# Optimization experiments

Hardware: AMD Instinct MI355X
Metric: run time of the kernel (lower is better)

Reference implementation:

```python
import jax, jax.numpy as jnp
import numpy as np

TOK_DIM, POS_DIM, HEAD_DIM = 3, 3, 64
D_MODEL, T, B = 128, 4096, 8


def setup_inputs() -> dict:
    key = jax.random.key(0)
    ks = jax.random.split(key, 8)
    s = 0.1
    return {
        "x": jax.random.normal(ks[0], (B, T, TOK_DIM + POS_DIM), jnp.float32),
        "Wq1": jax.random.normal(ks[1], (TOK_DIM, HEAD_DIM), jnp.float32) * s,
        "Wk1": jax.random.normal(ks[2], (TOK_DIM, HEAD_DIM), jnp.float32) * s,
        "Wv1": jax.random.normal(ks[3], (TOK_DIM, HEAD_DIM), jnp.float32) * s,
        "Wq2": jax.random.normal(ks[4], (POS_DIM, HEAD_DIM), jnp.float32) * s,
        "Wk2": jax.random.normal(ks[5], (POS_DIM, HEAD_DIM), jnp.float32) * s,
        "Wv2": jax.random.normal(ks[6], (POS_DIM, HEAD_DIM), jnp.float32) * s,
        "Wout": jax.random.normal(ks[7], (2 * HEAD_DIM, D_MODEL), jnp.float32) * s,
    }


def _attend(q, k, v):
    # q,k,v: [B,T,HEAD_DIM]; causal scaled dot-product attention
    scale = 1.0 / np.sqrt(HEAD_DIM).astype(np.float32)
    scores = jnp.einsum('btd,bsd->bts', q, k) * scale  # [B,T,T]
    t = scores.shape[1]
    causal = jnp.arange(t)[:, None] >= jnp.arange(t)[None, :]
    scores = jnp.where(causal[None], scores, -jnp.inf)
    p = jax.nn.softmax(scores, axis=-1)
    return jnp.einsum('bts,bsd->btd', p, v)


def reference(x, Wq1, Wk1, Wv1, Wq2, Wk2, Wv2, Wout):
    x_tok = x[:, :, :TOK_DIM]
    x_pos = x[:, :, TOK_DIM:]
    out1 = _attend(x_tok @ Wq1, x_tok @ Wk1, x_tok @ Wv1)
    out2 = _attend(x_pos @ Wq2, x_pos @ Wk2, x_pos @ Wv2)
    out = jnp.concatenate([out1, out2], axis=-1)  # [B,T,2*HEAD_DIM]
    return out @ Wout  # [B,T,D_MODEL]
```

## Files before the change

### kernel.cpp

```cpp
#include <hip/hip_runtime.h>
#include <hip/hip_bf16.h>
#include <stdint.h>

#define T_SEQ 4096

typedef float  f32x4   __attribute__((ext_vector_type(4)));
typedef float  f32x16  __attribute__((ext_vector_type(16)));
typedef short  bf16x8  __attribute__((ext_vector_type(8)));
typedef unsigned int u32x4 __attribute__((ext_vector_type(4)));

typedef const __attribute__((address_space(1))) uint32_t* gptr_t;
typedef __attribute__((address_space(3))) uint32_t* lptr_t;

__device__ __forceinline__ uint32_t f2bf1(float f) {
    uint32_t u = __float_as_uint(f);
    return (u + 0x7fffu + ((u >> 16) & 1u)) >> 16;
}
__device__ __forceinline__ short f2bfs(float f) { return (short)f2bf1(f); }
__device__ __forceinline__ uint32_t cvtpk(float lo, float hi) {
    uint32_t r;
    asm("v_cvt_pk_bf16_f32 %0, %1, %2" : "=v"(r) : "v"(lo), "v"(hi));
    return r;
}

__global__ __launch_bounds__(256) void qk_proj(
    const float* __restrict__ x,
    const float* __restrict__ Wq1, const float* __restrict__ Wk1,
    const float* __restrict__ Wq2, const float* __restrict__ Wk2,
    short* __restrict__ Q, short* __restrict__ K)
{
    int idx = blockIdx.x * 256 + threadIdx.x;
    int d = idx & 63;
    int t = (idx >> 6) & (T_SEQ - 1);
    int b = idx >> 18;
    const float* xp = x + (size_t)(b * T_SEQ + t) * 6;
    float x0 = xp[0], x1 = xp[1], x2 = xp[2];
    float x3 = xp[3], x4 = xp[4], x5 = xp[5];
    const float QS = 0.125f * 1.44269504088896340736f;
    float q1 = (x0 * Wq1[d] + x1 * Wq1[64 + d] + x2 * Wq1[128 + d]) * QS;
    float k1 =  x0 * Wk1[d] + x1 * Wk1[64 + d] + x2 * Wk1[128 + d];
    float q2 = (x3 * Wq2[d] + x4 * Wq2[64 + d] + x5 * Wq2[128 + d]) * QS;
    float k2 =  x3 * Wk2[d] + x4 * Wk2[64 + d] + x5 * Wk2[128 + d];
    size_t base1 = ((size_t)(b * 2 + 0) * T_SEQ + t) * 64 + d;
    size_t base2 = ((size_t)(b * 2 + 1) * T_SEQ + t) * 64 + d;
    Q[base1] = f2bfs(q1);  Q[base2] = f2bfs(q2);
    K[base1] = f2bfs(k1);  K[base2] = f2bfs(k2);
}

__global__ __launch_bounds__(256) void v_proj_t(
    const float* __restrict__ x,
    const float* __restrict__ Wv1, const float* __restrict__ Wv2,
    short* __restrict__ Vt)
{
    int bh = blockIdx.x >> 6;
    int tt = blockIdx.x & 63;
    int head = bh & 1, b = bh >> 1;
    int t  = tt * 64 + (threadIdx.x & 63);
    int dg = threadIdx.x >> 6;
    const float* Wv = head ? Wv2 : Wv1;
    const float* xp = x + (size_t)(b * T_SEQ + t) * 6 + head * 3;
    float x0 = xp[0], x1 = xp[1], x2 = xp[2];
    size_t base = (size_t)bh * 64 * T_SEQ + t;
    #pragma unroll
    for (int k = 0; k < 16; ++k) {
        int d = dg * 16 + k;
        float v = x0 * Wv[d] + x1 * Wv[64 + d] + x2 * Wv[128 + d];
        Vt[base + (size_t)d * T_SEQ] = f2bfs(v);
    }
}

__global__ __launch_bounds__(256, 4) void attn(
    const short* __restrict__ Q, const short* __restrict__ K,
    const short* __restrict__ Vt, float* __restrict__ Hf,
    float* __restrict__ P1, float* __restrict__ L0, float* __restrict__ L1)
{
    __shared__ __align__(16) char smem[32768];

    int id = blockIdx.x;
    int xcd = id & 7, rest = id >> 3;
    int bh = xcd * 2 + (rest & 1);
    int rem = rest >> 1;
    int s  = 63 - (rem >> 1);
    int p  = rem & 1;
    int tid = threadIdx.x;
    int W = tid >> 6;
    int lane = tid & 63;
    int ql = lane & 31, h = lane >> 5;
    int tile = W >> 1, half = W & 1;
    int t0 = 64 * s + 32 * tile;
    int q  = t0 + ql;
    int n  = s + 1;
    int nb = (n - p + 1) >> 1;

    size_t kvbase = (size_t)bh * (T_SEQ * 64);

    bf16x8 qf[4];
    #pragma unroll
    for (int ks = 0; ks < 4; ++ks)
        qf[ks] = *(const bf16x8*)(Q + kvbase + (size_t)q * 64 + ks * 16 + h * 8);

    int krl = tid >> 3;
    int kcol = ((tid & 7) ^ (krl & 7)) * 8;
    const short* ksrc0 = K + kvbase + kcol;
    const short* vsrc0 = Vt + kvbase + kcol;

    f32x16 acc0, acc1;
    #pragma unroll
    for (int rr = 0; rr < 16; ++rr) { acc0[rr] = 0.f; acc1[rr] = 0.f; }
    float l = 0.f;
    int swz = (ql & 7) << 4;

#define STAGE(bsel, kvv)                                                        \
    {                                                                           \
        char* kb = smem + (bsel) * 16384;                                       \
        char* vb = kb + 8192;                                                   \
        _Pragma("unroll")                                                       \
        for (int z = 0; z < 2; ++z)                                             \
            __builtin_amdgcn_global_load_lds(                                   \
                (gptr_t)(ksrc0 + (size_t)((kvv) + 32 * z + krl) * 64),          \
                (lptr_t)(kb + z * 4096 + tid * 16), 16, 0, 0);                  \
        _Pragma("unroll")                                                       \
        for (int z = 0; z < 2; ++z)                                             \
            __builtin_amdgcn_global_load_lds(                                   \
                (gptr_t)(vsrc0 + (size_t)(32 * z + krl) * T_SEQ + (kvv)),       \
                (lptr_t)(vb + z * 4096 + tid * 16), 16, 0, 0);                  \
    }

#define QK_SM(pf0, pf1)                                                         \
        {                                                                       \
            f32x16 Sv;                                                          \
            _Pragma("unroll") for (int rr = 0; rr < 16; ++rr) Sv[rr] = 0.f;     \
            Sv = __builtin_amdgcn_mfma_f32_32x32x16_bf16(kf0, qf[0], Sv,0,0,0); \
            Sv = __builtin_amdgcn_mfma_f32_32x32x16_bf16(kf1, qf[1], Sv,0,0,0); \
            Sv = __builtin_amdgcn_mfma_f32_32x32x16_bf16(kf2, qf[2], Sv,0,0,0); \
            Sv = __builtin_amdgcn_mfma_f32_32x32x16_bf16(kf3, qf[3], Sv,0,0,0); \
            bool needmask = (kv0 + 32 * half + 31 > t0);       \
            uint32_t pw[8];                                                     \
            float l0 = 0.f, l1 = 0.f;                                           \
            _Pragma("unroll") for (int e = 0; e < 8; ++e) {                     \
                float p0 = __builtin_amdgcn_exp2f(Sv[2 * e]);                   \
                float p1 = __builtin_amdgcn_exp2f(Sv[2 * e + 1]);               \
                if (needmask) {                                                 \
                    int kv = kv0 + 32 * half + 4 * h + 2 * (e & 1) + 8 * (e >> 1); \
                    p0 = (kv     <= q) ? p0 : 0.f;                              \
                    p1 = (kv + 1 <= q) ? p1 : 0.f;                              \
                }                                                               \
                l0 += p0; l1 += p1;                                             \
                pw[e] = cvtpk(p0, p1);                                          \
            }                                                                   \
            l += l0 + l1;                                                       \
            {                                                                   \
                uint32_t a0 = pw[0], b0 = pw[2], a1 = pw[1], b1 = pw[3];        \
                asm("v_permlane32_swap_b32 %0, %1" : "+v"(a0), "+v"(b0));       \
                asm("v_permlane32_swap_b32 %0, %1" : "+v"(a1), "+v"(b1));       \
                u32x4 fr = {a0, a1, b0, b1};                                    \
                pf0 = __builtin_bit_cast(bf16x8, fr);                           \
                uint32_t c0 = pw[4], d0 = pw[6], c1 = pw[5], d1 = pw[7];        \
                asm("v_permlane32_swap_b32 %0, %1" : "+v"(c0), "+v"(d0));       \
                asm("v_permlane32_swap_b32 %0, %1" : "+v"(c1), "+v"(d1));       \
                u32x4 fr1 = {c0, c1, d0, d1};                                   \
                pf1 = __builtin_bit_cast(bf16x8, fr1);                          \
            }                                                                   \
        }

#define BODY(jj)                                                                \
    {                                                                           \
        const int kv0 = 64 * (p + 2 * (jj));                                    \
        if ((jj) + 1 < nb) STAGE(((jj) + 1) & 1, kv0 + 128);                    \
        const char* kb = smem + ((jj) & 1) * 16384;                             \
        const char* vb = kb + 8192;                                             \
        const char* krw = kb + (32 * half + ql) * 128;                          \
        bf16x8 kf0 = *(const bf16x8*)(krw + ((0 * 32 + h * 16) ^ swz));         \
        bf16x8 kf1 = *(const bf16x8*)(krw + ((1 * 32 + h * 16) ^ swz));         \
        bf16x8 kf2 = *(const bf16x8*)(krw + ((2 * 32 + h * 16) ^ swz));         \
        bf16x8 kf3 = *(const bf16x8*)(krw + ((3 * 32 + h * 16) ^ swz));         \
        bool act = (kv0 + 32 * half <= t0 + 31);                                \
        bf16x8 pf0, pf1;                                                        \
        __builtin_amdgcn_s_setprio(1);                                          \
        if (act) QK_SM(pf0, pf1)                                                \
        const char* vr0 = vb + ql * 128;                                        \
        const char* vr1 = vb + (32 + ql) * 128;                                 \
        int vc0 = (64 * half + 16 * h) ^ swz;                                   \
        int vc1 = (64 * half + 32 + 16 * h) ^ swz;                              \
        bf16x8 vf00 = *(const bf16x8*)(vr0 + vc0);                              \
        bf16x8 vf01 = *(const bf16x8*)(vr0 + vc1);                              \
        bf16x8 vf10 = *(const bf16x8*)(vr1 + vc0);                              \
        bf16x8 vf11 = *(const bf16x8*)(vr1 + vc1);                              \
        if (act) {                                                              \
            acc0 = __builtin_amdgcn_mfma_f32_32x32x16_bf16(vf00, pf0, acc0, 0, 0, 0); \
            acc0 = __builtin_amdgcn_mfma_f32_32x32x16_bf16(vf01, pf1, acc0, 0, 0, 0); \
            acc1 = __builtin_amdgcn_mfma_f32_32x32x16_bf16(vf10, pf0, acc1, 0, 0, 0); \
            acc1 = __builtin_amdgcn_mfma_f32_32x32x16_bf16(vf11, pf1, acc1, 0, 0, 0); \
        }                                                                       \
        __builtin_amdgcn_s_setprio(0);                                          \
        __syncthreads();                                                        \
    }

    if (nb > 0) STAGE(0, 64 * p);
    __syncthreads();

    for (int j = 0; j < nb; ++j) BODY(j);
#undef BODY
#undef QK_SM
#undef STAGE

    l += __shfl_xor(l, 32);
    float* sg = (float*)smem + tile * 2112 + lane * 33;
    if (half == 1) {
        #pragma unroll
        for (int g = 0; g < 4; ++g) {
            *(f32x4*)(sg + 4 * g)      = f32x4{acc0[4*g+0], acc0[4*g+1], acc0[4*g+2], acc0[4*g+3]};
            *(f32x4*)(sg + 16 + 4 * g) = f32x4{acc1[4*g+0], acc1[4*g+1], acc1[4*g+2], acc1[4*g+3]};
        }
        sg[32] = l;
    }
    __syncthreads();
    if (half == 0) {
        #pragma unroll
        for (int g = 0; g < 4; ++g) {
            f32x4 u0 = *(f32x4*)(sg + 4 * g);
            f32x4 u1 = *(f32x4*)(sg + 16 + 4 * g);
            acc0[4*g+0] += u0[0]; acc0[4*g+1] += u0[1]; acc0[4*g+2] += u0[2]; acc0[4*g+3] += u0[3];
            acc1[4*g+0] += u1[0]; acc1[4*g+1] += u1[1]; acc1[4*g+2] += u1[2]; acc1[4*g+3] += u1[3];
        }
        l += sg[32];
        int head = bh & 1, bb = bh >> 1;
        float* Pdst = p ? P1 : Hf;
        float* Ldst = p ? L1 : L0;
        float* hp = Pdst + ((size_t)(bb * T_SEQ) + t0 + ql) * 128 + head * 64 + 4 * h;
        #pragma unroll
        for (int g2 = 0; g2 < 4; ++g2) {
            f32x4 s0 = { acc0[g2*4+0], acc0[g2*4+1], acc0[g2*4+2], acc0[g2*4+3] };
            *(f32x4*)(hp + 8 * g2) = s0;
            f32x4 s1 = { acc1[g2*4+0], acc1[g2*4+1], acc1[g2*4+2], acc1[g2*4+3] };
            *(f32x4*)(hp + 32 + 8 * g2) = s1;
        }
        if (h == 0)
            Ldst[(size_t)bh * T_SEQ + t0 + ql] = l;
    }
}

__global__ __launch_bounds__(256) void prep_wt(
    const float* __restrict__ Wout, short* __restrict__ Wt)
{
    int tid = blockIdx.x * 256 + threadIdx.x;
    int j = tid >> 7, k = tid & 127;
    float v = Wout[k * 128 + j];
    int slot = k >> 3;
    Wt[j * 128 + (((slot ^ (j & 7)) << 3) | (k & 7))] = f2bfs(v);
}

__global__ __launch_bounds__(256) void out_proj(
    const float* P0, const float* __restrict__ P1,
    const float* __restrict__ L0, const float* __restrict__ L1,
    const short* __restrict__ Wt, float* out)
{
    __shared__ __align__(16) char lws[32768];
    int tid = threadIdx.x;
    int w = tid >> 6, lane = tid & 63, c = lane & 15, g = lane >> 4;
    int cs = c & 7;
    #pragma unroll
    for (int z = 0; z < 8; ++z)
        __builtin_amdgcn_global_load_lds((gptr_t)(Wt + z * 2048 + w * 512 + lane * 8),
                                         (lptr_t)(lws + z * 4096 + w * 1024), 16, 0, 0);
    __syncthreads();

    int row0 = blockIdx.x * 64 + w * 16;
    int r = row0 + c;
    int b = r >> 12, t = r & (T_SEQ - 1);
    float rl0 = 1.0f / (L0[(size_t)(b * 2 + 0) * T_SEQ + t] + L1[(size_t)(b * 2 + 0) * T_SEQ + t]);
    float rl1 = 1.0f / (L0[(size_t)(b * 2 + 1) * T_SEQ + t] + L1[(size_t)(b * 2 + 1) * T_SEQ + t]);

    bf16x8 af[4];
    const float* hp0 = P0 + (size_t)r * 128 + g * 8;
    const float* hp1 = P1 + (size_t)r * 128 + g * 8;
    #pragma unroll
    for (int kc = 0; kc < 4; ++kc) {
        float rl = (kc < 2) ? rl0 : rl1;
        f32x4 x0 = *(const f32x4*)(hp0 + kc * 32);
        f32x4 x1 = *(const f32x4*)(hp0 + kc * 32 + 4);
        f32x4 y0 = *(const f32x4*)(hp1 + kc * 32);
        f32x4 y1 = *(const f32x4*)(hp1 + kc * 32 + 4);
        u32x4 wv = { cvtpk((x0[0]+y0[0])*rl, (x0[1]+y0[1])*rl),
                     cvtpk((x0[2]+y0[2])*rl, (x0[3]+y0[3])*rl),
                     cvtpk((x1[0]+y1[0])*rl, (x1[1]+y1[1])*rl),
                     cvtpk((x1[2]+y1[2])*rl, (x1[3]+y1[3])*rl) };
        af[kc] = __builtin_bit_cast(bf16x8, wv);
    }
    #pragma unroll
    for (int jt = 0; jt < 8; ++jt) {
        f32x4 accum = {0.f, 0.f, 0.f, 0.f};
        #pragma unroll
        for (int kc = 0; kc < 4; ++kc) {
            int row = jt * 16 + c;
            bf16x8 bfr = *(const bf16x8*)(lws + row * 256 + (((kc * 4 + g) ^ cs) << 4));
            accum = __builtin_amdgcn_mfma_f32_16x16x32_bf16(af[kc], bfr, accum, 0, 0, 0);
        }
        #pragma unroll
        for (int rr = 0; rr < 4; ++rr)
            out[(size_t)(row0 + g * 4 + rr) * 128 + jt * 16 + c] = accum[rr];
    }
}

extern "C" void kernel_launch(void* const* d_in, const int* in_sizes, int n_in,
                              void* d_out, int out_size, void* d_ws, size_t ws_size,
                              hipStream_t stream)
{
    (void)in_sizes; (void)n_in; (void)out_size; (void)ws_size;
    const float* x    = (const float*)d_in[0];
    const float* Wq1  = (const float*)d_in[1];
    const float* Wk1  = (const float*)d_in[2];
    const float* Wv1  = (const float*)d_in[3];
    const float* Wq2  = (const float*)d_in[4];
    const float* Wk2  = (const float*)d_in[5];
    const float* Wv2  = (const float*)d_in[6];
    const float* Wout = (const float*)d_in[7];
    float* out = (float*)d_out;

    char* ws = (char*)d_ws;
    short* Q  = (short*)(ws);
    short* K  = (short*)(ws + (size_t)8  * 1024 * 1024);
    short* Vt = (short*)(ws + (size_t)16 * 1024 * 1024);
    float* P1 = (float*)(ws + (size_t)24 * 1024 * 1024);
    float* L0 = (float*)(ws + (size_t)40 * 1024 * 1024);
    float* L1 = (float*)(ws + (size_t)40 * 1024 * 1024 + 262144);
    short* Wt = Q;
    float* Hf = out;

    qk_proj <<<8192, 256, 0, stream>>>(x, Wq1, Wk1, Wq2, Wk2, Q, K);
    v_proj_t<<<1024, 256, 0, stream>>>(x, Wv1, Wv2, Vt);
    attn    <<<2048, 256, 0, stream>>>(Q, K, Vt, Hf, P1, L0, L1);
    prep_wt <<<  64, 256, 0, stream>>>(Wout, Wt);
    out_proj<<< 512, 256, 0, stream>>>(Hf, P1, L0, L1, Wt, out);
}
```

Measured before the change: 89.08 us.

## Halve attention block to two waves each handling both query tiles

The attention kernel now runs 128-thread blocks of two waves instead of four. Each wave owns one 32-key half of the staged KV block and computes QK/softmax/PV for both the even and odd 32-row query tiles, so every K fragment loaded from LDS feeds two query tiles. The aim is to cut LDS reads per MFMA and improve reuse of the staged K/V data. In exchange, accumulator registers double (four f32x16 per wave), occupancy drops to a launch bound of 3, and each thread issues twice as many staging loads.

```diff
diff --git a/kernel.cpp b/kernel.cpp
--- a/kernel.cpp
+++ b/kernel.cpp
@@ -69,7 +69,7 @@
     }
 }
 
-__global__ __launch_bounds__(256, 4) void attn(
+__global__ __launch_bounds__(128, 3) void attn(
     const short* __restrict__ Q, const short* __restrict__ K,
     const short* __restrict__ Vt, float* __restrict__ Hf,
     float* __restrict__ P1, float* __restrict__ L0, float* __restrict__ L1)
@@ -80,75 +80,71 @@
     int xcd = id & 7, rest = id >> 3;
     int bh = xcd * 2 + (rest & 1);
     int rem = rest >> 1;
-    int s  = 63 - (rem >> 1);
+    int m  = 63 - (rem >> 1);
     int p  = rem & 1;
     int tid = threadIdx.x;
     int W = tid >> 6;
     int lane = tid & 63;
     int ql = lane & 31, h = lane >> 5;
-    int tile = W >> 1, half = W & 1;
-    int t0 = 64 * s + 32 * tile;
-    int q  = t0 + ql;
-    int n  = s + 1;
-    int nb = (n - p + 1) >> 1;
+    int t0E = 64 * m, t0O = t0E + 32;
+    int qE = t0E + ql, qO = t0O + ql;
+    int nb = (m + 2 - p) >> 1;
+    int head = bh & 1, bb = bh >> 1;
 
     size_t kvbase = (size_t)bh * (T_SEQ * 64);
 
-    bf16x8 qf[4];
-    #pragma unroll
-    for (int ks = 0; ks < 4; ++ks)
-        qf[ks] = *(const bf16x8*)(Q + kvbase + (size_t)q * 64 + ks * 16 + h * 8);
-
-    int krl = tid >> 3;
-    int kcol = ((tid & 7) ^ (krl & 7)) * 8;
-    const short* ksrc0 = K + kvbase + kcol;
-    const short* vsrc0 = Vt + kvbase + kcol;
-
-    f32x16 acc0, acc1;
-    #pragma unroll
-    for (int rr = 0; rr < 16; ++rr) { acc0[rr] = 0.f; acc1[rr] = 0.f; }
-    float l = 0.f;
+    bf16x8 qfE[4], qfO[4];
+    #pragma unroll
+    for (int ks = 0; ks < 4; ++ks) {
+        qfE[ks] = *(const bf16x8*)(Q + kvbase + (size_t)qE * 64 + ks * 16 + h * 8);
+        qfO[ks] = *(const bf16x8*)(Q + kvbase + (size_t)qO * 64 + ks * 16 + h * 8);
+    }
+
+    int row16 = tid >> 3;
+    int scol = ((tid & 7) ^ (row16 & 7)) * 8;
+    const short* ksrc = K  + kvbase + (size_t)row16 * 64 + scol;
+    const short* vsrc = Vt + kvbase + (size_t)row16 * T_SEQ + scol;
+
+    f32x16 accE0, accE1, accO0, accO1;
+    #pragma unroll
+    for (int r = 0; r < 16; ++r) { accE0[r]=0.f; accE1[r]=0.f; accO0[r]=0.f; accO1[r]=0.f; }
+    float lE = 0.f, lO = 0.f;
     int swz = (ql & 7) << 4;
 
-#define STAGE(bsel, kvv)                                                        \
-    {                                                                           \
-        char* kb = smem + (bsel) * 16384;                                       \
-        char* vb = kb + 8192;                                                   \
-        _Pragma("unroll")                                                       \
-        for (int z = 0; z < 2; ++z)                                             \
-            __builtin_amdgcn_global_load_lds(                                   \
-                (gptr_t)(ksrc0 + (size_t)((kvv) + 32 * z + krl) * 64),          \
-                (lptr_t)(kb + z * 4096 + tid * 16), 16, 0, 0);                  \
-        _Pragma("unroll")                                                       \
-        for (int z = 0; z < 2; ++z)                                             \
-            __builtin_amdgcn_global_load_lds(                                   \
-                (gptr_t)(vsrc0 + (size_t)(32 * z + krl) * T_SEQ + (kvv)),       \
-                (lptr_t)(vb + z * 4096 + tid * 16), 16, 0, 0);                  \
-    }
-
-#define QK_SM(pf0, pf1)                                                         \
+#define STAGE(nb_, kvv)                                                         \
+    _Pragma("unroll")                                                           \
+    for (int z = 0; z < 4; ++z) {                                               \
+        __builtin_amdgcn_global_load_lds(                                       \
+            (gptr_t)(ksrc + (size_t)((kvv) + z * 16) * 64),                     \
+            (lptr_t)((nb_) + z * 2048 + W * 1024), 16, 0, 0);                   \
+        __builtin_amdgcn_global_load_lds(                                       \
+            (gptr_t)(vsrc + (size_t)(z * 16) * T_SEQ + (kvv)),                  \
+            (lptr_t)((nb_) + 8192 + z * 2048 + W * 1024), 16, 0, 0);            \
+    }
+
+#define QK_SM(qfX, qX, lX, pf0, pf1)                                            \
         {                                                                       \
             f32x16 Sv;                                                          \
-            _Pragma("unroll") for (int rr = 0; rr < 16; ++rr) Sv[rr] = 0.f;     \
-            Sv = __builtin_amdgcn_mfma_f32_32x32x16_bf16(kf0, qf[0], Sv,0,0,0); \
-            Sv = __builtin_amdgcn_mfma_f32_32x32x16_bf16(kf1, qf[1], Sv,0,0,0); \
-            Sv = __builtin_amdgcn_mfma_f32_32x32x16_bf16(kf2, qf[2], Sv,0,0,0); \
-            Sv = __builtin_amdgcn_mfma_f32_32x32x16_bf16(kf3, qf[3], Sv,0,0,0); \
-            bool needmask = (kv0 + 32 * half + 31 > t0);       \
+            _Pragma("unroll") for (int r = 0; r < 16; ++r) Sv[r] = 0.f;         \
+            Sv = __builtin_amdgcn_mfma_f32_32x32x16_bf16(kf0, qfX[0], Sv,0,0,0);\
+            Sv = __builtin_amdgcn_mfma_f32_32x32x16_bf16(kf1, qfX[1], Sv,0,0,0);\
+            Sv = __builtin_amdgcn_mfma_f32_32x32x16_bf16(kf2, qfX[2], Sv,0,0,0);\
+            Sv = __builtin_amdgcn_mfma_f32_32x32x16_bf16(kf3, qfX[3], Sv,0,0,0);\
+            bool needmask = (kv0 + 32 * W + 31 > (qX) - ql);    \
             uint32_t pw[8];                                                     \
             float l0 = 0.f, l1 = 0.f;                                           \
             _Pragma("unroll") for (int e = 0; e < 8; ++e) {                     \
                 float p0 = __builtin_amdgcn_exp2f(Sv[2 * e]);                   \
                 float p1 = __builtin_amdgcn_exp2f(Sv[2 * e + 1]);               \
                 if (needmask) {                                                 \
-                    int kv = kv0 + 32 * half + 4 * h + 2 * (e & 1) + 8 * (e >> 1); \
-                    p0 = (kv     <= q) ? p0 : 0.f;                              \
-                    p1 = (kv + 1 <= q) ? p1 : 0.f;                              \
+                    int kv = kv0 + 32 * W + 4 * h + 2 * (e & 1) + 8 * (e >> 1); \
+                    p0 = (kv     <= (qX)) ? p0 : 0.f;                           \
+                    p1 = (kv + 1 <= (qX)) ? p1 : 0.f;                           \
                 }                                                               \
                 l0 += p0; l1 += p1;                                             \
                 pw[e] = cvtpk(p0, p1);                                          \
             }                                                                   \
-            l += l0 + l1;                                                       \
+            lX += l0 + l1;                                                      \
             {                                                                   \
                 uint32_t a0 = pw[0], b0 = pw[2], a1 = pw[1], b1 = pw[3];        \
                 asm("v_permlane32_swap_b32 %0, %1" : "+v"(a0), "+v"(b0));       \
@@ -166,37 +162,43 @@
 #define BODY(jj)                                                                \
     {                                                                           \
         const int kv0 = 64 * (p + 2 * (jj));                                    \
-        if ((jj) + 1 < nb) STAGE(((jj) + 1) & 1, kv0 + 128);                    \
-        const char* kb = smem + ((jj) & 1) * 16384;                             \
-        const char* vb = kb + 8192;                                             \
-        const char* krw = kb + (32 * half + ql) * 128;                          \
-        bf16x8 kf0 = *(const bf16x8*)(krw + ((0 * 32 + h * 16) ^ swz));         \
-        bf16x8 kf1 = *(const bf16x8*)(krw + ((1 * 32 + h * 16) ^ swz));         \
-        bf16x8 kf2 = *(const bf16x8*)(krw + ((2 * 32 + h * 16) ^ swz));         \
-        bf16x8 kf3 = *(const bf16x8*)(krw + ((3 * 32 + h * 16) ^ swz));         \
-        bool act = (kv0 + 32 * half <= t0 + 31);                                \
-        bf16x8 pf0, pf1;                                                        \
+        if ((jj) + 1 < nb) { char* nb_ = smem + (((jj) + 1) & 1) * 16384; STAGE(nb_, kv0 + 128); } \
+        const char* ldsK = smem + ((jj) & 1) * 16384;                           \
+        const char* ldsV = ldsK + 8192;                                         \
+        bool actE = (kv0 + 32 * W <= t0E + 31);                                 \
+        bool actO = (kv0 + 32 * W <= t0O + 31);                                 \
+        const char* krow = ldsK + (32 * W + ql) * 128;                          \
+        bf16x8 kf0 = *(const bf16x8*)(krow + ((0 * 32 + h * 16) ^ swz));        \
+        bf16x8 kf1 = *(const bf16x8*)(krow + ((1 * 32 + h * 16) ^ swz));        \
+        bf16x8 kf2 = *(const bf16x8*)(krow + ((2 * 32 + h * 16) ^ swz));        \
+        bf16x8 kf3 = *(const bf16x8*)(krow + ((3 * 32 + h * 16) ^ swz));        \
+        bf16x8 pfE0, pfE1, pfO0, pfO1;                                          \
         __builtin_amdgcn_s_setprio(1);                                          \
-        if (act) QK_SM(pf0, pf1)                                                \
-        const char* vr0 = vb + ql * 128;                                        \
-        const char* vr1 = vb + (32 + ql) * 128;                                 \
-        int vc0 = (64 * half + 16 * h) ^ swz;                                   \
-        int vc1 = (64 * half + 32 + 16 * h) ^ swz;                              \
-        bf16x8 vf00 = *(const bf16x8*)(vr0 + vc0);                              \
-        bf16x8 vf01 = *(const bf16x8*)(vr0 + vc1);                              \
-        bf16x8 vf10 = *(const bf16x8*)(vr1 + vc0);                              \
-        bf16x8 vf11 = *(const bf16x8*)(vr1 + vc1);                              \
-        if (act) {                                                              \
-            acc0 = __builtin_amdgcn_mfma_f32_32x32x16_bf16(vf00, pf0, acc0, 0, 0, 0); \
-            acc0 = __builtin_amdgcn_mfma_f32_32x32x16_bf16(vf01, pf1, acc0, 0, 0, 0); \
-            acc1 = __builtin_amdgcn_mfma_f32_32x32x16_bf16(vf10, pf0, acc1, 0, 0, 0); \
-            acc1 = __builtin_amdgcn_mfma_f32_32x32x16_bf16(vf11, pf1, acc1, 0, 0, 0); \
+        if (actO) QK_SM(qfO, qO, lO, pfO0, pfO1)                                \
+        if (actE) QK_SM(qfE, qE, lE, pfE0, pfE1)                                \
+        int cb0 = (2 * W + 0) * 32 + h * 16;                                    \
+        int cb1 = (2 * W + 1) * 32 + h * 16;                                    \
+        bf16x8 vf00 = *(const bf16x8*)(ldsV + ql * 128        + (cb0 ^ swz));   \
+        bf16x8 vf01 = *(const bf16x8*)(ldsV + ql * 128        + (cb1 ^ swz));   \
+        bf16x8 vf10 = *(const bf16x8*)(ldsV + (32 + ql) * 128 + (cb0 ^ swz));   \
+        bf16x8 vf11 = *(const bf16x8*)(ldsV + (32 + ql) * 128 + (cb1 ^ swz));   \
+        if (actO) {                                                             \
+            accO0 = __builtin_amdgcn_mfma_f32_32x32x16_bf16(vf00, pfO0, accO0, 0, 0, 0); \
+            accO0 = __builtin_amdgcn_mfma_f32_32x32x16_bf16(vf01, pfO1, accO0, 0, 0, 0); \
+            accO1 = __builtin_amdgcn_mfma_f32_32x32x16_bf16(vf10, pfO0, accO1, 0, 0, 0); \
+            accO1 = __builtin_amdgcn_mfma_f32_32x32x16_bf16(vf11, pfO1, accO1, 0, 0, 0); \
+        }                                                                       \
+        if (actE) {                                                             \
+            accE0 = __builtin_amdgcn_mfma_f32_32x32x16_bf16(vf00, pfE0, accE0, 0, 0, 0); \
+            accE0 = __builtin_amdgcn_mfma_f32_32x32x16_bf16(vf01, pfE1, accE0, 0, 0, 0); \
+            accE1 = __builtin_amdgcn_mfma_f32_32x32x16_bf16(vf10, pfE0, accE1, 0, 0, 0); \
+            accE1 = __builtin_amdgcn_mfma_f32_32x32x16_bf16(vf11, pfE1, accE1, 0, 0, 0); \
         }                                                                       \
         __builtin_amdgcn_s_setprio(0);                                          \
         __syncthreads();                                                        \
     }
 
-    if (nb > 0) STAGE(0, 64 * p);
+    if (nb > 0) STAGE(smem, 64 * p);
     __syncthreads();
 
     for (int j = 0; j < nb; ++j) BODY(j);
@@ -204,39 +206,50 @@
 #undef QK_SM
 #undef STAGE
 
-    l += __shfl_xor(l, 32);
-    float* sg = (float*)smem + tile * 2112 + lane * 33;
-    if (half == 1) {
+    lE += __shfl_xor(lE, 32);
+    lO += __shfl_xor(lO, 32);
+    float* RE = (float*)smem;
+    float* RO = RE + 2112;
+    if (W == 0) {
+        float* pb = RO + lane * 33;
         #pragma unroll
         for (int g = 0; g < 4; ++g) {
-            *(f32x4*)(sg + 4 * g)      = f32x4{acc0[4*g+0], acc0[4*g+1], acc0[4*g+2], acc0[4*g+3]};
-            *(f32x4*)(sg + 16 + 4 * g) = f32x4{acc1[4*g+0], acc1[4*g+1], acc1[4*g+2], acc1[4*g+3]};
-        }
-        sg[32] = l;
+            *(f32x4*)(pb + 4 * g)      = f32x4{accO0[4*g+0], accO0[4*g+1], accO0[4*g+2], accO0[4*g+3]};
+            *(f32x4*)(pb + 16 + 4 * g) = f32x4{accO1[4*g+0], accO1[4*g+1], accO1[4*g+2], accO1[4*g+3]};
+        }
+        pb[32] = lO;
+    } else {
+        float* pb = RE + lane * 33;
+        #pragma unroll
+        for (int g = 0; g < 4; ++g) {
+            *(f32x4*)(pb + 4 * g)      = f32x4{accE0[4*g+0], accE0[4*g+1], accE0[4*g+2], accE0[4*g+3]};
+            *(f32x4*)(pb + 16 + 4 * g) = f32x4{accE1[4*g+0], accE1[4*g+1], accE1[4*g+2], accE1[4*g+3]};
+        }
+        pb[32] = lE;
     }
     __syncthreads();
-    if (half == 0) {
-        #pragma unroll
-        for (int g = 0; g < 4; ++g) {
-            f32x4 u0 = *(f32x4*)(sg + 4 * g);
-            f32x4 u1 = *(f32x4*)(sg + 16 + 4 * g);
-            acc0[4*g+0] += u0[0]; acc0[4*g+1] += u0[1]; acc0[4*g+2] += u0[2]; acc0[4*g+3] += u0[3];
-            acc1[4*g+0] += u1[0]; acc1[4*g+1] += u1[1]; acc1[4*g+2] += u1[2]; acc1[4*g+3] += u1[3];
-        }
-        l += sg[32];
-        int head = bh & 1, bb = bh >> 1;
+    {
         float* Pdst = p ? P1 : Hf;
         float* Ldst = p ? L1 : L0;
+        float* pb = (W ? RO : RE) + lane * 33;
+        f32x16 a0 = W ? accO0 : accE0;
+        f32x16 a1 = W ? accO1 : accE1;
+        float lf = (W ? lO : lE) + pb[32];
+        int t0 = W ? t0O : t0E;
         float* hp = Pdst + ((size_t)(bb * T_SEQ) + t0 + ql) * 128 + head * 64 + 4 * h;
         #pragma unroll
         for (int g2 = 0; g2 < 4; ++g2) {
-            f32x4 s0 = { acc0[g2*4+0], acc0[g2*4+1], acc0[g2*4+2], acc0[g2*4+3] };
+            f32x4 o0 = *(f32x4*)(pb + g2 * 4);
+            f32x4 o1 = *(f32x4*)(pb + 16 + g2 * 4);
+            f32x4 s0 = { a0[g2*4+0]+o0[0], a0[g2*4+1]+o0[1],
+                         a0[g2*4+2]+o0[2], a0[g2*4+3]+o0[3] };
             *(f32x4*)(hp + 8 * g2) = s0;
-            f32x4 s1 = { acc1[g2*4+0], acc1[g2*4+1], acc1[g2*4+2], acc1[g2*4+3] };
+            f32x4 s1 = { a1[g2*4+0]+o1[0], a1[g2*4+1]+o1[1],
+                         a1[g2*4+2]+o1[2], a1[g2*4+3]+o1[3] };
             *(f32x4*)(hp + 32 + 8 * g2) = s1;
         }
         if (h == 0)
-            Ldst[(size_t)bh * T_SEQ + t0 + ql] = l;
+            Ldst[(size_t)bh * T_SEQ + t0 + ql] = lf;
     }
 }
 
@@ -329,7 +342,7 @@
 
     qk_proj <<<8192, 256, 0, stream>>>(x, Wq1, Wk1, Wq2, Wk2, Q, K);
     v_proj_t<<<1024, 256, 0, stream>>>(x, Wv1, Wv2, Vt);
-    attn    <<<2048, 256, 0, stream>>>(Q, K, Vt, Hf, P1, L0, L1);
+    attn    <<<2048, 128, 0, stream>>>(Q, K, Vt, Hf, P1, L0, L1);
     prep_wt <<<  64, 256, 0, stream>>>(Wout, Wt);
     out_proj<<< 512, 256, 0, stream>>>(Hf, P1, L0, L1, Wt, out);
 }
```

Measured after the change: 96.30 us. +8.1%, slower.

## Pre-swizzle V into MFMA fragment layout and load directly to registers

Applied to the files above, without the earlier changes.

The V projection kernel now writes V in a per-64-key-chunk layout that matches the MFMA operand fragments each lane needs. The attention kernel then loads V fragments straight from global memory into registers, double-buffered across iterations by a two-way unrolled loop, instead of staging V through LDS. This halves the LDS footprint and removes the LDS reads for V, which may allow more resident blocks. In exchange it adds global-load latency that depends on register prefetching and raises register pressure.

```diff
diff --git a/kernel.cpp b/kernel.cpp
--- a/kernel.cpp
+++ b/kernel.cpp
@@ -50,7 +50,7 @@
 __global__ __launch_bounds__(256) void v_proj_t(
     const float* __restrict__ x,
     const float* __restrict__ Wv1, const float* __restrict__ Wv2,
-    short* __restrict__ Vt)
+    short* __restrict__ Vf)
 {
     int bh = blockIdx.x >> 6;
     int tt = blockIdx.x & 63;
@@ -60,12 +60,16 @@
     const float* Wv = head ? Wv2 : Wv1;
     const float* xp = x + (size_t)(b * T_SEQ + t) * 6 + head * 3;
     float x0 = xp[0], x1 = xp[1], x2 = xp[2];
-    size_t base = (size_t)bh * 64 * T_SEQ + t;
+    int c = t >> 6, half = (t >> 5) & 1, kvq = t & 31;
+    int kvhi = kvq >> 4, hp = (kvq >> 3) & 1, e = kvq & 7;
+    size_t segbase = ((size_t)(bh * 64 + c) * 2 + half) * 2048;
     #pragma unroll
     for (int k = 0; k < 16; ++k) {
         int d = dg * 16 + k;
         float v = x0 * Wv[d] + x1 * Wv[64 + d] + x2 * Wv[128 + d];
-        Vt[base + (size_t)d * T_SEQ] = f2bfs(v);
+        int m = 2 * (d >> 5) + kvhi;
+        int l = (d & 31) + 32 * hp;
+        Vf[segbase + m * 512 + l * 8 + e] = f2bfs(v);
     }
 }
 
@@ -74,7 +78,7 @@
     const short* __restrict__ Vt, float* __restrict__ Hf,
     float* __restrict__ P1, float* __restrict__ L0, float* __restrict__ L1)
 {
-    __shared__ __align__(16) char smem[32768];
+    __shared__ __align__(16) char smem[17408];
 
     int id = blockIdx.x;
     int xcd = id & 7, rest = id >> 3;
@@ -102,7 +106,6 @@
     int krl = tid >> 3;
     int kcol = ((tid & 7) ^ (krl & 7)) * 8;
     const short* ksrc0 = K + kvbase + kcol;
-    const short* vsrc0 = Vt + kvbase + kcol;
 
     f32x16 acc0, acc1;
     #pragma unroll
@@ -112,18 +115,22 @@
 
 #define STAGE(bsel, kvv)                                                        \
     {                                                                           \
-        char* kb = smem + (bsel) * 16384;                                       \
-        char* vb = kb + 8192;                                                   \
+        char* kb = smem + (bsel) * 8192;                                        \
         _Pragma("unroll")                                                       \
         for (int z = 0; z < 2; ++z)                                             \
             __builtin_amdgcn_global_load_lds(                                   \
                 (gptr_t)(ksrc0 + (size_t)((kvv) + 32 * z + krl) * 64),          \
                 (lptr_t)(kb + z * 4096 + tid * 16), 16, 0, 0);                  \
-        _Pragma("unroll")                                                       \
-        for (int z = 0; z < 2; ++z)                                             \
-            __builtin_amdgcn_global_load_lds(                                   \
-                (gptr_t)(vsrc0 + (size_t)(32 * z + krl) * T_SEQ + (kvv)),       \
-                (lptr_t)(vb + z * 4096 + tid * 16), 16, 0, 0);                  \
+    }
+
+#define VLOAD(v0, v1, v2, v3, cc)                                               \
+    {                                                                           \
+        const short* vs = Vt + ((size_t)(bh * 64 + (cc)) * 2 + half) * 2048     \
+                             + lane * 8;                                        \
+        v0 = *(const bf16x8*)(vs);                                              \
+        v1 = *(const bf16x8*)(vs + 512);                                        \
+        v2 = *(const bf16x8*)(vs + 1024);                                       \
+        v3 = *(const bf16x8*)(vs + 1536);                                       \
     }
 
 #define QK_SM(pf0, pf1)                                                         \
@@ -163,12 +170,14 @@
             }                                                                   \
         }
 
-#define BODY(jj)                                                                \
+#define BODY(jj, va0, va1, va2, va3, vb0, vb1, vb2, vb3)                        \
     {                                                                           \
         const int kv0 = 64 * (p + 2 * (jj));                                    \
-        if ((jj) + 1 < nb) STAGE(((jj) + 1) & 1, kv0 + 128);                    \
-        const char* kb = smem + ((jj) & 1) * 16384;                             \
-        const char* vb = kb + 8192;                                             \
+        if ((jj) + 1 < nb) {                                                    \
+            STAGE(((jj) + 1) & 1, kv0 + 128);                                   \
+            VLOAD(vb0, vb1, vb2, vb3, p + 2 * ((jj) + 1));                      \
+        }                                                                       \
+        const char* kb = smem + ((jj) & 1) * 8192;                              \
         const char* krw = kb + (32 * half + ql) * 128;                          \
         bf16x8 kf0 = *(const bf16x8*)(krw + ((0 * 32 + h * 16) ^ swz));         \
         bf16x8 kf1 = *(const bf16x8*)(krw + ((1 * 32 + h * 16) ^ swz));         \
@@ -178,30 +187,30 @@
         bf16x8 pf0, pf1;                                                        \
         __builtin_amdgcn_s_setprio(1);                                          \
         if (act) QK_SM(pf0, pf1)                                                \
-        const char* vr0 = vb + ql * 128;                                        \
-        const char* vr1 = vb + (32 + ql) * 128;                                 \
-        int vc0 = (64 * half + 16 * h) ^ swz;                                   \
-        int vc1 = (64 * half + 32 + 16 * h) ^ swz;                              \
-        bf16x8 vf00 = *(const bf16x8*)(vr0 + vc0);                              \
-        bf16x8 vf01 = *(const bf16x8*)(vr0 + vc1);                              \
-        bf16x8 vf10 = *(const bf16x8*)(vr1 + vc0);                              \
-        bf16x8 vf11 = *(const bf16x8*)(vr1 + vc1);                              \
         if (act) {                                                              \
-            acc0 = __builtin_amdgcn_mfma_f32_32x32x16_bf16(vf00, pf0, acc0, 0, 0, 0); \
-            acc0 = __builtin_amdgcn_mfma_f32_32x32x16_bf16(vf01, pf1, acc0, 0, 0, 0); \
-            acc1 = __builtin_amdgcn_mfma_f32_32x32x16_bf16(vf10, pf0, acc1, 0, 0, 0); \
-            acc1 = __builtin_amdgcn_mfma_f32_32x32x16_bf16(vf11, pf1, acc1, 0, 0, 0); \
+            acc0 = __builtin_amdgcn_mfma_f32_32x32x16_bf16(va0, pf0, acc0, 0, 0, 0); \
+            acc0 = __builtin_amdgcn_mfma_f32_32x32x16_bf16(va1, pf1, acc0, 0, 0, 0); \
+            acc1 = __builtin_amdgcn_mfma_f32_32x32x16_bf16(va2, pf0, acc1, 0, 0, 0); \
+            acc1 = __builtin_amdgcn_mfma_f32_32x32x16_bf16(va3, pf1, acc1, 0, 0, 0); \
         }                                                                       \
         __builtin_amdgcn_s_setprio(0);                                          \
         __syncthreads();                                                        \
     }
 
-    if (nb > 0) STAGE(0, 64 * p);
+    bf16x8 vA0, vA1, vA2, vA3, vB0, vB1, vB2, vB3;
+    if (nb > 0) { STAGE(0, 64 * p); VLOAD(vA0, vA1, vA2, vA3, p); }
     __syncthreads();
 
-    for (int j = 0; j < nb; ++j) BODY(j);
+    int j = 0;
+    if (nb > 0) for (;;) {
+        BODY(j, vA0, vA1, vA2, vA3, vB0, vB1, vB2, vB3);
+        if (++j >= nb) break;
+        BODY(j, vB0, vB1, vB2, vB3, vA0, vA1, vA2, vA3);
+        if (++j >= nb) break;
+    }
 #undef BODY
 #undef QK_SM
+#undef VLOAD
 #undef STAGE
 
     l += __shfl_xor(l, 32);
@@ -320,7 +329,7 @@
     char* ws = (char*)d_ws;
     short* Q  = (short*)(ws);
     short* K  = (short*)(ws + (size_t)8  * 1024 * 1024);
-    short* Vt = (short*)(ws + (size_t)16 * 1024 * 1024);
+    short* Vf = (short*)(ws + (size_t)16 * 1024 * 1024);
     float* P1 = (float*)(ws + (size_t)24 * 1024 * 1024);
     float* L0 = (float*)(ws + (size_t)40 * 1024 * 1024);
     float* L1 = (float*)(ws + (size_t)40 * 1024 * 1024 + 262144);
@@ -328,8 +337,8 @@
     float* Hf = out;
 
     qk_proj <<<8192, 256, 0, stream>>>(x, Wq1, Wk1, Wq2, Wk2, Q, K);
-    v_proj_t<<<1024, 256, 0, stream>>>(x, Wv1, Wv2, Vt);
-    attn    <<<2048, 256, 0, stream>>>(Q, K, Vt, Hf, P1, L0, L1);
+    v_proj_t<<<1024, 256, 0, stream>>>(x, Wv1, Wv2, Vf);
+    attn    <<<2048, 256, 0, stream>>>(Q, K, Vf, Hf, P1, L0, L1);
     prep_wt <<<  64, 256, 0, stream>>>(Wout, Wt);
     out_proj<<< 512, 256, 0, stream>>>(Hf, P1, L0, L1, Wt, out);
 }
```

New measurement: 150.6 us. 69.1% more time.
